# Kernel optimization log

Measured on AMD Instinct MI355X. Metric: run time of the kernel, lower is better.

## Reference

```python
import jax, jax.numpy as jnp
import numpy as np

NUM_HEADS = 2
POOL_K = 256
REPEAT = 20


def setup_inputs() -> dict:
    key = jax.random.key(0)
    k1, k2, k3 = jax.random.split(key, 3)
    C = 6144
    d = C // NUM_HEADS                      # 3072
    N = REPEAT * (d // POOL_K)              # 240, required by Pq add
    x = jax.random.normal(k1, (N, C), dtype=jnp.float32)
    w_qkv = jax.random.normal(k2, (3 * C, C), dtype=jnp.float32) * 0.02
    w_proj = jax.random.normal(k3, (C, C), dtype=jnp.float32) * 0.02
    b_proj = jnp.zeros((C,), dtype=jnp.float32)
    return {"x": x, "w_qkv": w_qkv, "w_proj": w_proj, "b_proj": b_proj}


def reference(x, w_qkv, w_proj, b_proj):
    N, C = x.shape
    H = NUM_HEADS
    d = C // H
    scale = d ** -0.5
    # qkv: (N, 3C) -> (N, 3, H, d) -> (3, H, N, d)
    qkv = (x @ w_qkv.T).reshape(N, 3, H, d).transpose(1, 2, 0, 3)
    q, k, v = qkv[0], qkv[1], qkv[2]        # each (H, N, d)
    # MaxPool1d(256) over last dim, then tile x20 along last dim -> (H, N, N)
    Pq = q.reshape(H, N, d // POOL_K, POOL_K).max(axis=-1)
    Pq = jnp.tile(Pq, (1, 1, REPEAT))       # (H, N, N)
    attn = jnp.einsum('hnd,hmd->hnm', q, k) * scale + 0.1 * Pq
    attn = jax.nn.softmax(attn, axis=-1)
    out = jnp.einsum('hnm,hmd->hnd', attn, v)    # (H, N, d)
    out = out.transpose(1, 0, 2).reshape(N, C)
    return out @ w_proj.T + b_proj
```

## Files before the change

kernel.cpp:

```cpp
#include <hip/hip_runtime.h>
#include <hip/hip_bf16.h>

#define NN 240
#define CC 6144
#define DD 3072
#define C3 18432
#define HH 2

typedef __attribute__((ext_vector_type(8))) short bf16x8;
typedef __attribute__((ext_vector_type(4))) float f32x4;
typedef unsigned short ushort_t;

static __device__ __forceinline__ unsigned short f2bf(float f) {
    __hip_bfloat16 h = __float2bfloat16(f);
    return __builtin_bit_cast(unsigned short, h);
}

#define GLDS16(g, l) __builtin_amdgcn_global_load_lds( \
    (const __attribute__((address_space(1))) void*)(g), \
    (__attribute__((address_space(3))) void*)(l), 16, 0, 0)

__global__ __launch_bounds__(256, 2)
void gemm_pb(const ushort_t* __restrict__ Ab, int lda,
             const float* __restrict__ B, int ldb,
             const float* __restrict__ bias,
             float* __restrict__ C0,
             float* __restrict__ CP, long long sCPz,
             int ldc, int N, int Kc, int KS,
             ushort_t* __restrict__ Qb) {
    __shared__ ushort_t sA[256 * 32];
    __shared__ float    sB[32 * 256];

    const int kc = blockIdx.z;
    const ushort_t* Abase = Ab + (size_t)kc * Kc;
    const float*    Bbase = B  + (size_t)kc * Kc;
    float* Cw = (kc == 0) ? C0 : (CP + (size_t)(kc - 1) * sCPz);

    const int n0 = blockIdx.x * 32;
    const int tid = threadIdx.x, lane = tid & 63, wid = tid >> 6;
    const int l16 = lane & 15, lk = lane >> 4;

    const int ar = lane >> 2;
    const int akoct = (lane & 3) ^ ((lane >> 3) & 3);

    const int nTot = Kc / 32;
    f32x4 acc[4][2] = {};

    auto ISSUE_A = [&](int t32) {
#pragma unroll
        for (int i = 0; i < 4; ++i) {
            int rb = (wid * 4 + i) * 16;
            GLDS16(Abase + (size_t)(rb + ar) * lda + akoct * 8
                       + (size_t)t32 * 32,
                   sA + rb * 32);
        }
    };
    auto ISSUE_B = [&](int T) {
#pragma unroll
        for (int i = 0; i < 8; ++i) {
            int c = wid * 8 + i;
            const float* src = Bbase + (size_t)(n0 + c) * ldb
                               + (size_t)T * 256 + (lane ^ i) * 4;
            GLDS16(src, sB + c * 256);
        }
    };
    auto COMPUTE = [&](int s) {
        bf16x8 af[4];
#pragma unroll
        for (int mt = 0; mt < 4; ++mt) {
            int r = wid * 64 + mt * 16 + l16;
            af[mt] = *(const bf16x8*)((const char*)sA + r * 64
                        + ((lk ^ ((r >> 1) & 3)) * 16));
        }
#pragma unroll
        for (int nf = 0; nf < 2; ++nf) {
            int c = nf * 16 + l16;
            int j0 = (s * 8 + 2 * lk) ^ (c & 7);
            int j1 = (s * 8 + 2 * lk + 1) ^ (c & 7);
            f32x4 lo = *(const f32x4*)(sB + c * 256 + j0 * 4);
            f32x4 hi = *(const f32x4*)(sB + c * 256 + j1 * 4);
            bf16x8 r;
            r[0] = (short)f2bf(lo[0]); r[1] = (short)f2bf(lo[1]);
            r[2] = (short)f2bf(lo[2]); r[3] = (short)f2bf(lo[3]);
            r[4] = (short)f2bf(hi[0]); r[5] = (short)f2bf(hi[1]);
            r[6] = (short)f2bf(hi[2]); r[7] = (short)f2bf(hi[3]);
#pragma unroll
            for (int mt = 0; mt < 4; ++mt)
                acc[mt][nf] = __builtin_amdgcn_mfma_f32_16x16x32_bf16(
                    af[mt], r, acc[mt][nf], 0, 0, 0);
        }
    };

    ISSUE_B(0);
    for (int t = 0; t < nTot; ++t) {
        ISSUE_A(t);
        __syncthreads();
        COMPUTE(t & 7);
        __syncthreads();
        if ((t & 7) == 7 && t + 1 < nTot)
            ISSUE_B((t >> 3) + 1);
    }

#pragma unroll
    for (int mt = 0; mt < 4; ++mt) {
#pragma unroll
        for (int j = 0; j < 4; ++j) {
            int grow = wid * 64 + mt * 16 + lk * 4 + j;
            if (grow < NN) {
#pragma unroll
                for (int nf = 0; nf < 2; ++nf) {
                    int gcol = n0 + nf * 16 + l16;
                    if (gcol < N) {
                        float v = acc[mt][nf][j];
                        if (kc == 0 && bias) v += bias[gcol];
                        Cw[(size_t)grow * ldc + gcol] = v;
                        if (Qb && gcol < CC)
                            Qb[(size_t)grow * CC + gcol] = f2bf(v);
                    }
                }
            }
        }
    }
}

__global__ __launch_bounds__(256, 4)
void gemm_m97(const ushort_t* __restrict__ Ab, int lda, long long sAz,
              const float* __restrict__ B, int ldb, long long sBz,
              float* __restrict__ C0, long long sC0z,
              float* __restrict__ CP, long long sCPz,
              int ldc, int N, int Kc, int KS) {
    __shared__ ushort_t sA[256 * 32];
    __shared__ float    sB[64 * 32];

    const int zc = blockIdx.z;
    const int z = zc / KS, kc = zc % KS;
    const ushort_t* Abase = Ab + (size_t)z * sAz + (size_t)kc * Kc;
    const float*    Bbase = B  + (size_t)z * sBz + (size_t)kc * Kc;
    float* Cw = (kc == 0) ? (C0 + (size_t)z * sC0z)
                          : (CP + (size_t)(z * (KS - 1) + kc - 1) * sCPz);

    const int n0 = blockIdx.x * 64;
    const int tid = threadIdx.x, lane = tid & 63, wid = tid >> 6;
    const int l16 = lane & 15, lk = lane >> 4;

    const int ar = lane >> 2;
    const int akoct = (lane & 3) ^ ((lane >> 3) & 3);

    long long bofs[2];
#pragma unroll
    for (int i = 0; i < 2; ++i) {
        int cl = (wid * 2 + i) * 8 + (lane >> 3);
        int cg = n0 + cl; if (cg > N - 1) cg = N - 1;
        bofs[i] = (long long)cg * ldb + ((lane & 7) ^ ((lane >> 3) & 7)) * 4;
    }

    const int nt = Kc / 32;
    f32x4 acc[4][4] = {};

    for (int t = 0; t < nt; ++t) {
#pragma unroll
        for (int i = 0; i < 4; ++i) {
            int rb = (wid * 4 + i) * 16;
            GLDS16(Abase + (size_t)(rb + ar) * lda + akoct * 8 + (size_t)t * 32,
                   sA + rb * 32);
        }
#pragma unroll
        for (int i = 0; i < 2; ++i) {
            int cb = (wid * 2 + i) * 8;
            GLDS16(Bbase + bofs[i] + (size_t)t * 32, sB + cb * 32);
        }
        __syncthreads();

        bf16x8 af[4];
#pragma unroll
        for (int mt = 0; mt < 4; ++mt) {
            int r = wid * 64 + mt * 16 + l16;
            af[mt] = *(const bf16x8*)((const char*)sA + r * 64
                        + ((lk ^ ((r >> 1) & 3)) * 16));
        }
#pragma unroll
        for (int nf = 0; nf < 4; ++nf) {
            int c = nf * 16 + l16;
            const char* cb = (const char*)sB + c * 128;
            f32x4 lo = *(const f32x4*)(cb + (((2 * lk) ^ (c & 7)) * 16));
            f32x4 hi = *(const f32x4*)(cb + (((2 * lk + 1) ^ (c & 7)) * 16));
            bf16x8 r;
            r[0] = (short)f2bf(lo[0]); r[1] = (short)f2bf(lo[1]);
            r[2] = (short)f2bf(lo[2]); r[3] = (short)f2bf(lo[3]);
            r[4] = (short)f2bf(hi[0]); r[5] = (short)f2bf(hi[1]);
            r[6] = (short)f2bf(hi[2]); r[7] = (short)f2bf(hi[3]);
#pragma unroll
            for (int mt = 0; mt < 4; ++mt)
                acc[mt][nf] = __builtin_amdgcn_mfma_f32_16x16x32_bf16(
                    af[mt], r, acc[mt][nf], 0, 0, 0);
        }
        __syncthreads();
    }

#pragma unroll
    for (int mt = 0; mt < 4; ++mt) {
#pragma unroll
        for (int j = 0; j < 4; ++j) {
            int grow = wid * 64 + mt * 16 + lk * 4 + j;
            if (grow < NN) {
#pragma unroll
                for (int nf = 0; nf < 4; ++nf) {
                    int gcol = n0 + nf * 16 + l16;
                    if (gcol < N)
                        Cw[(size_t)grow * ldc + gcol] = acc[mt][nf][j];
                }
            }
        }
    }
}

__global__ __launch_bounds__(256)
void convert_kernel(const float* __restrict__ x, ushort_t* __restrict__ xb) {
    int id = blockIdx.x * 256 + threadIdx.x;
    int row = id / 768, c8 = id % 768;
    bf16x8 o = {};
    if (row < NN) {
        const float* p = x + (size_t)row * CC + c8 * 8;
        float4 a = *(const float4*)p, b = *(const float4*)(p + 4);
        o[0] = (short)f2bf(a.x); o[1] = (short)f2bf(a.y);
        o[2] = (short)f2bf(a.z); o[3] = (short)f2bf(a.w);
        o[4] = (short)f2bf(b.x); o[5] = (short)f2bf(b.y);
        o[6] = (short)f2bf(b.z); o[7] = (short)f2bf(b.w);
    }
    *(bf16x8*)(xb + (size_t)row * CC + c8 * 8) = o;
}

__global__ __launch_bounds__(256)
void reduce_proj(float4* __restrict__ o4, const float4* __restrict__ p4,
                 long long s4) {
    int i = blockIdx.x * 256 + threadIdx.x;
    float4 a = o4[i];
#pragma unroll
    for (int k = 0; k < 3; ++k) {
        float4 b = p4[(size_t)k * s4 + i];
        a.x += b.x; a.y += b.y; a.z += b.z; a.w += b.w;
    }
    o4[i] = a;
}

__global__ __launch_bounds__(256)
void qmax_kernel(const float* __restrict__ qkv, float* __restrict__ qmax) {
    int idx = blockIdx.x * 4 + (threadIdx.x >> 6);
    int lane = threadIdx.x & 63;
    int c = idx % 12;
    int r = idx / 12;
    int n = r % NN, h = r / NN;
    const float* p = qkv + (size_t)n * C3 + h * DD + c * 256 + lane * 4;
    float4 f = *(const float4*)p;
    float m = fmaxf(fmaxf(f.x, f.y), fmaxf(f.z, f.w));
#pragma unroll
    for (int off = 32; off >= 1; off >>= 1)
        m = fmaxf(m, __shfl_xor(m, off));
    if (lane == 0) qmax[idx] = m;
}

__global__ __launch_bounds__(256)
void softmax_kernel(float* __restrict__ attn, const float* __restrict__ gpart,
                    int ksm1, const float* __restrict__ qmax) {
    int r = blockIdx.x * 4 + (threadIdx.x >> 6);
    int lane = threadIdx.x & 63;
    int z = r / NN, n = r % NN;
    float* row = attn + (size_t)r * NN;
    const float* qm = qmax + r * 12;
    const float scale = 0.0180421959f;
    float v[4];
    float mx = -1e30f;
#pragma unroll
    for (int i = 0; i < 4; ++i) {
        int m = lane + 64 * i;
        v[i] = -1e30f;
        if (m < NN) {
            float s = row[m];
            for (int kc = 0; kc < ksm1; ++kc)
                s += gpart[(size_t)(z * ksm1 + kc) * (NN * NN)
                           + (size_t)n * NN + m];
            v[i] = s * scale + 0.1f * qm[m % 12];
        }
        mx = fmaxf(mx, v[i]);
    }
#pragma unroll
    for (int off = 32; off >= 1; off >>= 1)
        mx = fmaxf(mx, __shfl_xor(mx, off));
    float s = 0.f;
#pragma unroll
    for (int i = 0; i < 4; ++i) {
        v[i] = __expf(v[i] - mx);
        s += v[i];
    }
#pragma unroll
    for (int off = 32; off >= 1; off >>= 1)
        s += __shfl_xor(s, off);
    float inv = 1.0f / s;
#pragma unroll
    for (int i = 0; i < 4; ++i) {
        int m = lane + 64 * i;
        if (m < NN) row[m] = v[i] * inv;
    }
}

__global__ __launch_bounds__(256)
void pv_kernel(const float* __restrict__ attn, const float* __restrict__ qkv,
               ushort_t* __restrict__ preb) {
    const int h = blockIdx.z;
    const int n0 = blockIdx.y * 16;
    const int dd0 = blockIdx.x * 256;
    __shared__ float s_attn[16 * NN];
    for (int i = threadIdx.x; i < 16 * NN; i += 256)
        s_attn[i] = attn[(size_t)h * NN * NN + (n0 + i / NN) * NN + (i % NN)];
    __syncthreads();

    const float* vp = qkv + 2 * CC + h * DD + dd0 + threadIdx.x;
    float acc[16] = {};
    for (int m = 0; m < NN; m += 4) {
        float v0 = vp[(size_t)(m + 0) * C3];
        float v1 = vp[(size_t)(m + 1) * C3];
        float v2 = vp[(size_t)(m + 2) * C3];
        float v3 = vp[(size_t)(m + 3) * C3];
#pragma unroll
        for (int i = 0; i < 16; ++i) {
            float4 a = *(const float4*)&s_attn[i * NN + m];
            acc[i] += a.x * v0 + a.y * v1 + a.z * v2 + a.w * v3;
        }
    }
#pragma unroll
    for (int i = 0; i < 16; ++i)
        preb[(size_t)(n0 + i) * CC + h * DD + dd0 + threadIdx.x] =
            f2bf(acc[i]);
}

extern "C" void kernel_launch(void* const* d_in, const int* in_sizes, int n_in,
                              void* d_out, int out_size, void* d_ws, size_t ws_size,
                              hipStream_t stream) {
    const float* x      = (const float*)d_in[0];
    const float* w_qkv  = (const float*)d_in[1];
    const float* w_proj = (const float*)d_in[2];
    const float* b_proj = (const float*)d_in[3];
    float* out = (float*)d_out;

    const size_t f_qkv  = (size_t)NN * C3;
    const size_t f_attn = (size_t)HH * NN * NN;
    const size_t f_qmax = (size_t)HH * NN * 12;
    const size_t f_pre  = (size_t)NN * CC;
    float* qkv   = (float*)d_ws;
    float* attn  = qkv + f_qkv;
    float* qmaxb = attn + f_attn;
    ushort_t* xb   = (ushort_t*)(qmaxb + f_qmax);
    ushort_t* qb   = xb + (size_t)256 * CC;
    ushort_t* preb = qb + (size_t)256 * CC;
    float* gpart = (float*)(preb + (size_t)256 * CC);

    convert_kernel<<<768, 256, 0, stream>>>(x, xb);

    gemm_pb<<<dim3(C3 / 32, 1, 1), 256, 0, stream>>>(
        xb, CC, w_qkv, CC, nullptr,
        qkv, nullptr, 0LL,
        C3, C3, CC, 1, qb);

    qmax_kernel<<<1440, 256, 0, stream>>>(qkv, qmaxb);

    gemm_m97<<<dim3(4, 1, HH * 24), 256, 0, stream>>>(
        qb, CC, (long long)DD,
        qkv + CC, C3, (long long)DD,
        attn, (long long)(NN * NN), gpart, (long long)(NN * NN),
        NN, NN, DD / 24, 24);

    softmax_kernel<<<120, 256, 0, stream>>>(attn, gpart, 23, qmaxb);

    pv_kernel<<<dim3(12, 15, HH), 256, 0, stream>>>(attn, qkv, preb);

    gemm_pb<<<dim3(CC / 32, 1, 4), 256, 0, stream>>>(
        preb, CC, w_proj, CC, b_proj,
        out, gpart, (long long)f_pre,
        CC, CC, CC / 4, 4, nullptr);
    reduce_proj<<<1440, 256, 0, stream>>>((float4*)out, (const float4*)gpart,
        (long long)(f_pre / 4));
}
```

Measured before the change: 350.9 us.

## Add producer-wavefront double-buffered B staging and widen GEMM column tile

Replaces the GEMM kernel with a warp-specialized version: a fifth wavefront acts as producer, prefetching the next fp32 weight tile into a double-buffered LDS slot while the four consumer waves compute. The column tile doubles to 64 per block, with the K chunk cut to 128, and each wave now loads its own private A slice, so the per-slice __syncthreads pairs become one barrier per 128-wide K tile. The aim is to hide weight-load latency and increase A reuse. In exchange the grid has half as many blocks, the accumulator is twice as large, and each consumer wave still waits on its own A loads synchronously.

Measured after the change: 467.3 us. 1.33x slower.

```diff
diff --git a/kernel.cpp b/kernel.cpp
--- a/kernel.cpp
+++ b/kernel.cpp
@@ -20,102 +20,123 @@
     (const __attribute__((address_space(1))) void*)(g), \
     (__attribute__((address_space(3))) void*)(l), 16, 0, 0)
 
-__global__ __launch_bounds__(256, 2)
-void gemm_pb(const ushort_t* __restrict__ Ab, int lda,
+__global__ __launch_bounds__(320, 2)
+void gemm_pc(const ushort_t* __restrict__ Ab, int lda,
              const float* __restrict__ B, int ldb,
              const float* __restrict__ bias,
              float* __restrict__ C0,
              float* __restrict__ CP, long long sCPz,
              int ldc, int N, int Kc, int KS,
              ushort_t* __restrict__ Qb) {
-    __shared__ ushort_t sA[256 * 32];
-    __shared__ float    sB[32 * 256];
+    __shared__ ushort_t sA[4][64 * 32];
+    __shared__ float    sB[2][64 * 128];
 
     const int kc = blockIdx.z;
     const ushort_t* Abase = Ab + (size_t)kc * Kc;
     const float*    Bbase = B  + (size_t)kc * Kc;
     float* Cw = (kc == 0) ? C0 : (CP + (size_t)(kc - 1) * sCPz);
 
-    const int n0 = blockIdx.x * 32;
+    const int n0 = blockIdx.x * 64;
     const int tid = threadIdx.x, lane = tid & 63, wid = tid >> 6;
     const int l16 = lane & 15, lk = lane >> 4;
+    const int nT = Kc / 128;
+    const bool producer = (wid == 4);
+
+    const int chalf = lane >> 5;
+    const int sl = lane & 31;
 
     const int ar = lane >> 2;
     const int akoct = (lane & 3) ^ ((lane >> 3) & 3);
 
-    const int nTot = Kc / 32;
-    f32x4 acc[4][2] = {};
-
-    auto ISSUE_A = [&](int t32) {
-#pragma unroll
-        for (int i = 0; i < 4; ++i) {
-            int rb = (wid * 4 + i) * 16;
-            GLDS16(Abase + (size_t)(rb + ar) * lda + akoct * 8
-                       + (size_t)t32 * 32,
-                   sA + rb * 32);
-        }
-    };
-    auto ISSUE_B = [&](int T) {
-#pragma unroll
-        for (int i = 0; i < 8; ++i) {
-            int c = wid * 8 + i;
-            const float* src = Bbase + (size_t)(n0 + c) * ldb
-                               + (size_t)T * 256 + (lane ^ i) * 4;
-            GLDS16(src, sB + c * 256);
-        }
-    };
-    auto COMPUTE = [&](int s) {
-        bf16x8 af[4];
+    f32x4 acc[4][4] = {};
+
+    if (producer) {
+#pragma unroll
+        for (int i = 0; i < 32; ++i) {
+            int col = 2 * i + chalf;
+            const float* src = Bbase + (size_t)(n0 + col) * ldb
+                               + ((sl ^ (col & 7)) * 4);
+            GLDS16(src, &sB[0][i * 256]);
+        }
+        asm volatile("s_waitcnt vmcnt(0)" ::: "memory");
+    }
+    __syncthreads();
+
+    for (int T = 0; T < nT; ++T) {
+        if (producer) {
+            if (T + 1 < nT) {
+#pragma unroll
+                for (int i = 0; i < 32; ++i) {
+                    int col = 2 * i + chalf;
+                    const float* src = Bbase + (size_t)(n0 + col) * ldb
+                                       + (size_t)(T + 1) * 128
+                                       + ((sl ^ (col & 7)) * 4);
+                    GLDS16(src, &sB[(T + 1) & 1][i * 256]);
+                }
+                asm volatile("s_waitcnt vmcnt(0)" ::: "memory");
+            }
+        } else {
+            const float* Bs = sB[T & 1];
+#pragma unroll
+            for (int s = 0; s < 4; ++s) {
+#pragma unroll
+                for (int i = 0; i < 4; ++i) {
+                    GLDS16(Abase + (size_t)(wid * 64 + i * 16 + ar) * lda
+                               + akoct * 8 + (size_t)(T * 4 + s) * 32,
+                           &sA[wid][i * 512]);
+                }
+                asm volatile("s_waitcnt vmcnt(0)" ::: "memory");
+                __builtin_amdgcn_sched_barrier(0);
+
+                bf16x8 af[4];
+#pragma unroll
+                for (int mt = 0; mt < 4; ++mt) {
+                    int lr = mt * 16 + l16;
+                    af[mt] = *(const bf16x8*)((const char*)sA[wid] + lr * 64
+                                + ((lk ^ ((lr >> 1) & 3)) * 16));
+                }
+#pragma unroll
+                for (int nf = 0; nf < 4; ++nf) {
+                    int c = nf * 16 + l16;
+                    int j0 = (s * 8 + 2 * lk) ^ (c & 7);
+                    int j1 = (s * 8 + 2 * lk + 1) ^ (c & 7);
+                    const char* cb = (const char*)(Bs + c * 128);
+                    f32x4 lo = *(const f32x4*)(cb + j0 * 16);
+                    f32x4 hi = *(const f32x4*)(cb + j1 * 16);
+                    bf16x8 r;
+                    r[0] = (short)f2bf(lo[0]); r[1] = (short)f2bf(lo[1]);
+                    r[2] = (short)f2bf(lo[2]); r[3] = (short)f2bf(lo[3]);
+                    r[4] = (short)f2bf(hi[0]); r[5] = (short)f2bf(hi[1]);
+                    r[6] = (short)f2bf(hi[2]); r[7] = (short)f2bf(hi[3]);
+#pragma unroll
+                    for (int mt = 0; mt < 4; ++mt)
+                        acc[mt][nf] = __builtin_amdgcn_mfma_f32_16x16x32_bf16(
+                            af[mt], r, acc[mt][nf], 0, 0, 0);
+                }
+                asm volatile("s_waitcnt lgkmcnt(0)" ::: "memory");
+                __builtin_amdgcn_sched_barrier(0);
+            }
+        }
+        __syncthreads();
+    }
+
+    if (!producer) {
 #pragma unroll
         for (int mt = 0; mt < 4; ++mt) {
-            int r = wid * 64 + mt * 16 + l16;
-            af[mt] = *(const bf16x8*)((const char*)sA + r * 64
-                        + ((lk ^ ((r >> 1) & 3)) * 16));
-        }
-#pragma unroll
-        for (int nf = 0; nf < 2; ++nf) {
-            int c = nf * 16 + l16;
-            int j0 = (s * 8 + 2 * lk) ^ (c & 7);
-            int j1 = (s * 8 + 2 * lk + 1) ^ (c & 7);
-            f32x4 lo = *(const f32x4*)(sB + c * 256 + j0 * 4);
-            f32x4 hi = *(const f32x4*)(sB + c * 256 + j1 * 4);
-            bf16x8 r;
-            r[0] = (short)f2bf(lo[0]); r[1] = (short)f2bf(lo[1]);
-            r[2] = (short)f2bf(lo[2]); r[3] = (short)f2bf(lo[3]);
-            r[4] = (short)f2bf(hi[0]); r[5] = (short)f2bf(hi[1]);
-            r[6] = (short)f2bf(hi[2]); r[7] = (short)f2bf(hi[3]);
-#pragma unroll
-            for (int mt = 0; mt < 4; ++mt)
-                acc[mt][nf] = __builtin_amdgcn_mfma_f32_16x16x32_bf16(
-                    af[mt], r, acc[mt][nf], 0, 0, 0);
-        }
-    };
-
-    ISSUE_B(0);
-    for (int t = 0; t < nTot; ++t) {
-        ISSUE_A(t);
-        __syncthreads();
-        COMPUTE(t & 7);
-        __syncthreads();
-        if ((t & 7) == 7 && t + 1 < nTot)
-            ISSUE_B((t >> 3) + 1);
-    }
-
-#pragma unroll
-    for (int mt = 0; mt < 4; ++mt) {
-#pragma unroll
-        for (int j = 0; j < 4; ++j) {
-            int grow = wid * 64 + mt * 16 + lk * 4 + j;
-            if (grow < NN) {
-#pragma unroll
-                for (int nf = 0; nf < 2; ++nf) {
-                    int gcol = n0 + nf * 16 + l16;
-                    if (gcol < N) {
-                        float v = acc[mt][nf][j];
-                        if (kc == 0 && bias) v += bias[gcol];
-                        Cw[(size_t)grow * ldc + gcol] = v;
-                        if (Qb && gcol < CC)
-                            Qb[(size_t)grow * CC + gcol] = f2bf(v);
+#pragma unroll
+            for (int j = 0; j < 4; ++j) {
+                int grow = wid * 64 + mt * 16 + lk * 4 + j;
+                if (grow < NN) {
+#pragma unroll
+                    for (int nf = 0; nf < 4; ++nf) {
+                        int gcol = n0 + nf * 16 + l16;
+                        if (gcol < N) {
+                            float v = acc[mt][nf][j];
+                            if (kc == 0 && bias) v += bias[gcol];
+                            Cw[(size_t)grow * ldc + gcol] = v;
+                            if (Qb && gcol < CC)
+                                Qb[(size_t)grow * CC + gcol] = f2bf(v);
+                        }
                     }
                 }
             }
@@ -356,7 +377,7 @@
 
     convert_kernel<<<768, 256, 0, stream>>>(x, xb);
 
-    gemm_pb<<<dim3(C3 / 32, 1, 1), 256, 0, stream>>>(
+    gemm_pc<<<dim3(C3 / 64, 1, 1), 320, 0, stream>>>(
         xb, CC, w_qkv, CC, nullptr,
         qkv, nullptr, 0LL,
         C3, C3, CC, 1, qb);
@@ -373,7 +394,7 @@
 
     pv_kernel<<<dim3(12, 15, HH), 256, 0, stream>>>(attn, qkv, preb);
 
-    gemm_pb<<<dim3(CC / 32, 1, 4), 256, 0, stream>>>(
+    gemm_pc<<<dim3(CC / 64, 1, 4), 320, 0, stream>>>(
         preb, CC, w_proj, CC, b_proj,
         out, gpart, (long long)f_pre,
         CC, CC, CC / 4, 4, nullptr);
```
